# Kernel tuning notes

Measured on AMD Instinct MI355X. Metric: run time of the kernel, lower is better.

Reference implementation:

```python
import jax, jax.numpy as jnp
import numpy as np

D_MODEL = 1024
NUM_HEADS = 16
DFF = 4096
DEPTH = D_MODEL // NUM_HEADS
EPS = 1e-6


def setup_inputs() -> dict:
    key = jax.random.key(0)
    ks = jax.random.split(key, 12)
    B, S, D = 4, 2048, D_MODEL
    scale = 0.02
    inp = {
        "x": jax.random.normal(ks[0], (B, S, D), dtype=jnp.float32),
        "mask": jnp.zeros((B, 1, 1, S), dtype=jnp.float32),
        "wq": jax.random.normal(ks[1], (D, D), dtype=jnp.float32) * scale,
        "bq": jnp.zeros((D,), dtype=jnp.float32),
        "wk": jax.random.normal(ks[2], (D, D), dtype=jnp.float32) * scale,
        "bk": jnp.zeros((D,), dtype=jnp.float32),
        "wv": jax.random.normal(ks[3], (D, D), dtype=jnp.float32) * scale,
        "bv": jnp.zeros((D,), dtype=jnp.float32),
        "wo": jax.random.normal(ks[4], (D, D), dtype=jnp.float32) * scale,
        "bo": jnp.zeros((D,), dtype=jnp.float32),
        "w1": jax.random.normal(ks[5], (D, DFF), dtype=jnp.float32) * scale,
        "b1": jnp.zeros((DFF,), dtype=jnp.float32),
        "w2": jax.random.normal(ks[6], (DFF, D), dtype=jnp.float32) * scale,
        "b2": jnp.zeros((D,), dtype=jnp.float32),
        "g1": jnp.ones((D,), dtype=jnp.float32),
        "beta1": jnp.zeros((D,), dtype=jnp.float32),
        "g2": jnp.ones((D,), dtype=jnp.float32),
        "beta2": jnp.zeros((D,), dtype=jnp.float32),
    }
    return inp


def _layernorm(x, gamma, beta):
    mu = jnp.mean(x, axis=-1, keepdims=True)
    var = jnp.mean(jnp.square(x - mu), axis=-1, keepdims=True)
    return (x - mu) * jax.lax.rsqrt(var + EPS) * gamma + beta


def _split_heads(t, B, S):
    # [B,S,D] -> [B,H,S,depth]
    return t.reshape(B, S, NUM_HEADS, DEPTH).transpose(0, 2, 1, 3)


def encoder_layer(x, mask, wq, bq, wk, bk, wv, bv, wo, bo,
                  w1, b1, w2, b2, g1, beta1, g2, beta2):
    B, S, D = x.shape
    q = _split_heads(x @ wq + bq, B, S)
    k = _split_heads(x @ wk + bk, B, S)
    v = _split_heads(x @ wv + bv, B, S)
    logits = jnp.einsum("bhqd,bhkd->bhqk", q, k) / jnp.sqrt(
        jnp.asarray(DEPTH, dtype=x.dtype))
    if mask is not None:
        logits = logits + mask * -1e9
    attn = jax.nn.softmax(logits, axis=-1)
    ctx = jnp.einsum("bhqk,bhkd->bhqd", attn, v)
    ctx = ctx.transpose(0, 2, 1, 3).reshape(B, S, D)
    attn_out = ctx @ wo + bo
    out1 = _layernorm(x + attn_out, g1, beta1)
    ffn = jax.nn.relu(out1 @ w1 + b1) @ w2 + b2
    out2 = _layernorm(out1 + ffn, g2, beta2)
    return out2


def reference(x, mask, wq, bq, wk, bk, wv, bv, wo, bo,
              w1, b1, w2, b2, g1, beta1, g2, beta2):
    return encoder_layer(x, mask, wq, bq, wk, bk, wv, bv, wo, bo,
                         w1, b1, w2, b2, g1, beta1, g2, beta2)
```

## Files before the change

kernel.cpp:

```cpp
#include <hip/hip_runtime.h>
#include <cstdint>


#define BATCH 4
#define SEQ   2048
#define DM    1024
#define NH    16
#define DEPTH 64
#define DFF_  4096
#define EPSF  1e-6f

typedef short bf16x8 __attribute__((ext_vector_type(8)));
typedef float f32x4  __attribute__((ext_vector_type(4)));

__device__ __forceinline__ unsigned short f2bf(float f) {
  union { float f; unsigned int u; } v; v.f = f;
  unsigned int u = v.u;
  return (unsigned short)((u + 0x7fffu + ((u >> 16) & 1u)) >> 16);
}

__device__ __forceinline__ void gload_lds16(const void* g, void* l) {
  __builtin_amdgcn_global_load_lds(
      (const __attribute__((address_space(1))) unsigned int*)g,
      (__attribute__((address_space(3))) unsigned int*)l, 16, 0, 0);
}

#define VMCNT(n) asm volatile("s_waitcnt vmcnt(" #n ")" ::: "memory")

template<int EPI>
__global__ __launch_bounds__(512, 2)
void gemm8(const unsigned short* __restrict__ A, const unsigned short* __restrict__ Bt,
           const float* __restrict__ bias0, const float* __restrict__ bias1,
           const float* __restrict__ bias2, float* __restrict__ Cf,
           unsigned short* __restrict__ Cb0, unsigned short* __restrict__ Cb1,
           unsigned short* __restrict__ Cb2, int M, int N, int K)
{
  __shared__ char smem[131072];
  const int tid  = threadIdx.x;
  const int lane = tid & 63;
  const int wid  = tid >> 6;
  const int wr   = wid >> 2;
  const int wcn  = wid & 3;
  const int fr   = lane & 15;
  const int kh   = lane >> 4;

  const int nbx  = N >> 8;
  const int nwg  = gridDim.x;
  const int flat = blockIdx.x;
  const int swz  = (flat & 7) * (nwg >> 3) + (flat >> 3);
  const int bx = swz % nbx, by = swz / nbx;
  const int m0 = by << 8, n0 = bx << 8;

  const int lr  = tid >> 3;
  const int ch  = tid & 7;
  const int sch = ch ^ (lr & 7);
  const char* gA = (const char*)A + ((size_t)(m0 + lr) * K) * 2 + sch * 16;
  const char* gB = (const char*)Bt + ((size_t)(n0 + lr) * K) * 2 + sch * 16;
  const size_t rstep = (size_t)K * 128;

  const int chk0 = ((kh) ^ (fr & 7)) * 16;
  const int chk1 = ((4 + kh) ^ (fr & 7)) * 16;
  const int rowA = wr * 128 + fr;
  const int rowB = wcn * 64 + fr;

  f32x4 acc[8][4] = {};
  bf16x8 bg[4][2];
  const int NT = K >> 6;

  {
    char* sb = smem;
    gload_lds16(gB + 0 * rstep, sb + 32768 + 0 * 8192 + tid * 16);
    gload_lds16(gB + 1 * rstep, sb + 32768 + 1 * 8192 + tid * 16);
    gload_lds16(gB + 2 * rstep, sb + 32768 + 2 * 8192 + tid * 16);
    gload_lds16(gB + 3 * rstep, sb + 32768 + 3 * 8192 + tid * 16);
    gload_lds16(gA + 0 * rstep, sb + 0 * 8192 + tid * 16);
    gload_lds16(gA + 2 * rstep, sb + 2 * 8192 + tid * 16);
    gload_lds16(gA + 1 * rstep, sb + 1 * 8192 + tid * 16);
    gload_lds16(gA + 3 * rstep, sb + 3 * 8192 + tid * 16);
    VMCNT(2);
    __builtin_amdgcn_s_barrier();
  }

  for (int t = 0; t < NT - 1; ++t) {
    char* rb = smem + ((t & 1) << 16);
    char* sb = smem + (((t + 1) & 1) << 16);
    const size_t kg = (size_t)(t + 1) * 128;
#pragma unroll
    for (int p = 0; p < 4; ++p) {
      if (p == 0) {
        gload_lds16(gB + kg + 0 * rstep, sb + 32768 + 0 * 8192 + tid * 16);
        gload_lds16(gB + kg + 1 * rstep, sb + 32768 + 1 * 8192 + tid * 16);
      } else if (p == 1) {
        gload_lds16(gB + kg + 2 * rstep, sb + 32768 + 2 * 8192 + tid * 16);
        gload_lds16(gB + kg + 3 * rstep, sb + 32768 + 3 * 8192 + tid * 16);
      } else if (p == 2) {
        gload_lds16(gA + kg + 0 * rstep, sb + 0 * 8192 + tid * 16);
        gload_lds16(gA + kg + 2 * rstep, sb + 2 * 8192 + tid * 16);
      } else {
        gload_lds16(gA + kg + 1 * rstep, sb + 1 * 8192 + tid * 16);
        gload_lds16(gA + kg + 3 * rstep, sb + 3 * 8192 + tid * 16);
      }
      if (p == 0) {
#pragma unroll
        for (int j = 0; j < 4; ++j) {
          bg[j][0] = *(const bf16x8*)(rb + 32768 + (rowB + j * 16) * 128 + chk0);
          bg[j][1] = *(const bf16x8*)(rb + 32768 + (rowB + j * 16) * 128 + chk1);
        }
      }
      bf16x8 a00 = *(const bf16x8*)(rb + (rowA + (2 * p) * 16) * 128 + chk0);
      bf16x8 a01 = *(const bf16x8*)(rb + (rowA + (2 * p) * 16) * 128 + chk1);
      bf16x8 a10 = *(const bf16x8*)(rb + (rowA + (2 * p + 1) * 16) * 128 + chk0);
      bf16x8 a11 = *(const bf16x8*)(rb + (rowA + (2 * p + 1) * 16) * 128 + chk1);
      __builtin_amdgcn_s_barrier();
      __builtin_amdgcn_s_setprio(1);
#pragma unroll
      for (int j = 0; j < 4; ++j) {
        acc[2*p][j]   = __builtin_amdgcn_mfma_f32_16x16x32_bf16(a00, bg[j][0], acc[2*p][j], 0, 0, 0);
        acc[2*p][j]   = __builtin_amdgcn_mfma_f32_16x16x32_bf16(a01, bg[j][1], acc[2*p][j], 0, 0, 0);
        acc[2*p+1][j] = __builtin_amdgcn_mfma_f32_16x16x32_bf16(a10, bg[j][0], acc[2*p+1][j], 0, 0, 0);
        acc[2*p+1][j] = __builtin_amdgcn_mfma_f32_16x16x32_bf16(a11, bg[j][1], acc[2*p+1][j], 0, 0, 0);
      }
      __builtin_amdgcn_s_setprio(0);
      if (p == 1) VMCNT(4);
      if (p == 3) VMCNT(2);
      __builtin_amdgcn_s_barrier();
    }
  }
  {
    char* rb = smem + (((NT - 1) & 1) << 16);
#pragma unroll
    for (int p = 0; p < 4; ++p) {
      if (p == 0) {
#pragma unroll
        for (int j = 0; j < 4; ++j) {
          bg[j][0] = *(const bf16x8*)(rb + 32768 + (rowB + j * 16) * 128 + chk0);
          bg[j][1] = *(const bf16x8*)(rb + 32768 + (rowB + j * 16) * 128 + chk1);
        }
      }
      bf16x8 a00 = *(const bf16x8*)(rb + (rowA + (2 * p) * 16) * 128 + chk0);
      bf16x8 a01 = *(const bf16x8*)(rb + (rowA + (2 * p) * 16) * 128 + chk1);
      bf16x8 a10 = *(const bf16x8*)(rb + (rowA + (2 * p + 1) * 16) * 128 + chk0);
      bf16x8 a11 = *(const bf16x8*)(rb + (rowA + (2 * p + 1) * 16) * 128 + chk1);
      __builtin_amdgcn_s_barrier();
      __builtin_amdgcn_s_setprio(1);
#pragma unroll
      for (int j = 0; j < 4; ++j) {
        acc[2*p][j]   = __builtin_amdgcn_mfma_f32_16x16x32_bf16(a00, bg[j][0], acc[2*p][j], 0, 0, 0);
        acc[2*p][j]   = __builtin_amdgcn_mfma_f32_16x16x32_bf16(a01, bg[j][1], acc[2*p][j], 0, 0, 0);
        acc[2*p+1][j] = __builtin_amdgcn_mfma_f32_16x16x32_bf16(a10, bg[j][0], acc[2*p+1][j], 0, 0, 0);
        acc[2*p+1][j] = __builtin_amdgcn_mfma_f32_16x16x32_bf16(a11, bg[j][1], acc[2*p+1][j], 0, 0, 0);
      }
      __builtin_amdgcn_s_setprio(0);
      if (p == 1) VMCNT(0);
      __builtin_amdgcn_s_barrier();
    }
  }

  if (EPI == 2) {
    const int seg = n0 >> 10;
    const float* bp = seg == 0 ? bias0 : (seg == 1 ? bias1 : bias2);
    unsigned short* dst = seg == 0 ? Cb0 : (seg == 1 ? Cb1 : Cb2);
    float bc[4];
#pragma unroll
    for (int j = 0; j < 4; ++j) bc[j] = bp[(n0 & 1023) + wcn * 64 + j * 16 + fr];
#pragma unroll
    for (int m = 0; m < 8; ++m)
#pragma unroll
      for (int jj = 0; jj < 4; ++jj) {
        const int row = m0 + wr * 128 + m * 16 + kh * 4 + jj;
        const int b = row >> 11, s = row & (SEQ - 1);
#pragma unroll
        for (int j = 0; j < 4; ++j) {
          const int cs = (n0 & 1023) + wcn * 64 + j * 16 + fr;
          const int hh = cs >> 6, d = cs & 63;
          const float v = acc[m][j][jj] + bc[j];
          if (seg < 2)
            dst[(((size_t)(b * NH + hh)) * SEQ + s) * DEPTH + d] = f2bf(v);
          else
            dst[(((size_t)(b * NH + hh)) * DEPTH + d) * SEQ + s] = f2bf(v);
        }
      }
  } else {
    float bc[4];
#pragma unroll
    for (int j = 0; j < 4; ++j) bc[j] = bias0[n0 + wcn * 64 + j * 16 + fr];
#pragma unroll
    for (int m = 0; m < 8; ++m)
#pragma unroll
      for (int jj = 0; jj < 4; ++jj) {
        const int row = m0 + wr * 128 + m * 16 + kh * 4 + jj;
#pragma unroll
        for (int j = 0; j < 4; ++j) {
          const int col = n0 + wcn * 64 + j * 16 + fr;
          float v = acc[m][j][jj] + bc[j];
          if (EPI == 1) {
            v = fmaxf(v, 0.f);
            Cb0[(size_t)row * N + col] = f2bf(v);
          } else {
            Cf[(size_t)row * N + col] = v;
          }
        }
      }
  }
}

template<int EPI>
__global__ __launch_bounds__(512, 2)
void gemm128(const unsigned short* __restrict__ A, const unsigned short* __restrict__ Bt,
             const float* __restrict__ bias0, const float* __restrict__ bias1,
             const float* __restrict__ bias2, float* __restrict__ Cf,
             unsigned short* __restrict__ Cb0, unsigned short* __restrict__ Cb1,
             unsigned short* __restrict__ Cb2, int M, int N, int K)
{
  __shared__ char smem[98304];
  const int tid  = threadIdx.x;
  const int lane = tid & 63;
  const int wid  = tid >> 6;
  const int fr   = lane & 15;
  const int kh   = lane >> 4;

  const int nbx  = N >> 8;
  const int nwg  = gridDim.x;
  const int flat = blockIdx.x;
  const int swz  = (flat & 7) * (nwg >> 3) + (flat >> 3);
  const int bx = swz % nbx, by = swz / nbx;
  const int m0 = by << 7, n0 = bx << 8;

  const int lr  = tid >> 3;
  const int sch = (tid & 7) ^ (lr & 7);
  const char* gA = (const char*)A + ((size_t)(m0 + lr) * K) * 2 + sch * 16;
  const char* gB = (const char*)Bt + ((size_t)(n0 + lr) * K) * 2 + sch * 16;
  const size_t rstep = (size_t)K * 128;

  const int chk0 = ((kh) ^ (fr & 7)) * 16;
  const int chk1 = ((4 + kh) ^ (fr & 7)) * 16;
  const int rowB = wid * 32 + fr;

  f32x4 acc[8][2] = {};
  bf16x8 bg[2][2];
  const int NT = K >> 6;

  {
    char* sb = smem;
    gload_lds16(gB + 0 * rstep, sb + 16384 + 0 * 8192 + tid * 16);
    gload_lds16(gB + 1 * rstep, sb + 16384 + 1 * 8192 + tid * 16);
    gload_lds16(gB + 2 * rstep, sb + 16384 + 2 * 8192 + tid * 16);
    gload_lds16(gB + 3 * rstep, sb + 16384 + 3 * 8192 + tid * 16);
    gload_lds16(gA + 0 * rstep, sb + 0 * 8192 + tid * 16);
    gload_lds16(gA + 1 * rstep, sb + 1 * 8192 + tid * 16);
    VMCNT(1);
    __builtin_amdgcn_s_barrier();
  }

  for (int t = 0; t < NT - 1; ++t) {
    char* rb = smem + (t & 1) * 49152;
    char* sb = smem + ((t + 1) & 1) * 49152;
    const size_t kg = (size_t)(t + 1) * 128;
#pragma unroll
    for (int p = 0; p < 4; ++p) {
      if (p == 0) {
        gload_lds16(gB + kg + 0 * rstep, sb + 16384 + 0 * 8192 + tid * 16);
        gload_lds16(gB + kg + 1 * rstep, sb + 16384 + 1 * 8192 + tid * 16);
      } else if (p == 1) {
        gload_lds16(gB + kg + 2 * rstep, sb + 16384 + 2 * 8192 + tid * 16);
        gload_lds16(gB + kg + 3 * rstep, sb + 16384 + 3 * 8192 + tid * 16);
      } else if (p == 2) {
        gload_lds16(gA + kg + 0 * rstep, sb + 0 * 8192 + tid * 16);
      } else {
        gload_lds16(gA + kg + 1 * rstep, sb + 1 * 8192 + tid * 16);
      }
      if (p == 0) {
#pragma unroll
        for (int j = 0; j < 2; ++j) {
          bg[j][0] = *(const bf16x8*)(rb + 16384 + (rowB + j * 16) * 128 + chk0);
          bg[j][1] = *(const bf16x8*)(rb + 16384 + (rowB + j * 16) * 128 + chk1);
        }
      }
      bf16x8 a00 = *(const bf16x8*)(rb + ((2 * p) * 16 + fr) * 128 + chk0);
      bf16x8 a01 = *(const bf16x8*)(rb + ((2 * p) * 16 + fr) * 128 + chk1);
      bf16x8 a10 = *(const bf16x8*)(rb + ((2 * p + 1) * 16 + fr) * 128 + chk0);
      bf16x8 a11 = *(const bf16x8*)(rb + ((2 * p + 1) * 16 + fr) * 128 + chk1);
      __builtin_amdgcn_s_barrier();
      __builtin_amdgcn_s_setprio(1);
#pragma unroll
      for (int j = 0; j < 2; ++j) {
        acc[2*p][j]   = __builtin_amdgcn_mfma_f32_16x16x32_bf16(a00, bg[j][0], acc[2*p][j], 0, 0, 0);
        acc[2*p][j]   = __builtin_amdgcn_mfma_f32_16x16x32_bf16(a01, bg[j][1], acc[2*p][j], 0, 0, 0);
        acc[2*p+1][j] = __builtin_amdgcn_mfma_f32_16x16x32_bf16(a10, bg[j][0], acc[2*p+1][j], 0, 0, 0);
        acc[2*p+1][j] = __builtin_amdgcn_mfma_f32_16x16x32_bf16(a11, bg[j][1], acc[2*p+1][j], 0, 0, 0);
      }
      __builtin_amdgcn_s_setprio(0);
      if (p == 1) VMCNT(4);
      if (p == 3) VMCNT(1);
      __builtin_amdgcn_s_barrier();
    }
  }
  {
    char* rb = smem + ((NT - 1) & 1) * 49152;
#pragma unroll
    for (int p = 0; p < 4; ++p) {
      if (p == 0) {
#pragma unroll
        for (int j = 0; j < 2; ++j) {
          bg[j][0] = *(const bf16x8*)(rb + 16384 + (rowB + j * 16) * 128 + chk0);
          bg[j][1] = *(const bf16x8*)(rb + 16384 + (rowB + j * 16) * 128 + chk1);
        }
      }
      bf16x8 a00 = *(const bf16x8*)(rb + ((2 * p) * 16 + fr) * 128 + chk0);
      bf16x8 a01 = *(const bf16x8*)(rb + ((2 * p) * 16 + fr) * 128 + chk1);
      bf16x8 a10 = *(const bf16x8*)(rb + ((2 * p + 1) * 16 + fr) * 128 + chk0);
      bf16x8 a11 = *(const bf16x8*)(rb + ((2 * p + 1) * 16 + fr) * 128 + chk1);
      __builtin_amdgcn_s_barrier();
      __builtin_amdgcn_s_setprio(1);
#pragma unroll
      for (int j = 0; j < 2; ++j) {
        acc[2*p][j]   = __builtin_amdgcn_mfma_f32_16x16x32_bf16(a00, bg[j][0], acc[2*p][j], 0, 0, 0);
        acc[2*p][j]   = __builtin_amdgcn_mfma_f32_16x16x32_bf16(a01, bg[j][1], acc[2*p][j], 0, 0, 0);
        acc[2*p+1][j] = __builtin_amdgcn_mfma_f32_16x16x32_bf16(a10, bg[j][0], acc[2*p+1][j], 0, 0, 0);
        acc[2*p+1][j] = __builtin_amdgcn_mfma_f32_16x16x32_bf16(a11, bg[j][1], acc[2*p+1][j], 0, 0, 0);
      }
      __builtin_amdgcn_s_setprio(0);
      if (p == 1) VMCNT(0);
      __builtin_amdgcn_s_barrier();
    }
  }

  if (EPI == 2) {
    const int seg = n0 >> 10;
    const float* bp = seg == 0 ? bias0 : (seg == 1 ? bias1 : bias2);
    unsigned short* dst = seg == 0 ? Cb0 : (seg == 1 ? Cb1 : Cb2);
    float bc[2];
#pragma unroll
    for (int j = 0; j < 2; ++j) bc[j] = bp[(n0 & 1023) + wid * 32 + j * 16 + fr];
#pragma unroll
    for (int m = 0; m < 8; ++m)
#pragma unroll
      for (int jj = 0; jj < 4; ++jj) {
        const int row = m0 + m * 16 + kh * 4 + jj;
        const int b = row >> 11, s = row & (SEQ - 1);
#pragma unroll
        for (int j = 0; j < 2; ++j) {
          const int cs = (n0 & 1023) + wid * 32 + j * 16 + fr;
          const int hh = cs >> 6, d = cs & 63;
          const float v = acc[m][j][jj] + bc[j];
          if (seg < 2)
            dst[(((size_t)(b * NH + hh)) * SEQ + s) * DEPTH + d] = f2bf(v);
          else
            dst[(((size_t)(b * NH + hh)) * DEPTH + d) * SEQ + s] = f2bf(v);
        }
      }
  } else {
    float bc[2];
#pragma unroll
    for (int j = 0; j < 2; ++j) bc[j] = bias0[n0 + wid * 32 + j * 16 + fr];
#pragma unroll
    for (int m = 0; m < 8; ++m)
#pragma unroll
      for (int jj = 0; jj < 4; ++jj) {
        const int row = m0 + m * 16 + kh * 4 + jj;
#pragma unroll
        for (int j = 0; j < 2; ++j) {
          const int col = n0 + wid * 32 + j * 16 + fr;
          Cf[(size_t)row * N + col] = acc[m][j][jj] + bc[j];
        }
      }
  }
}

__global__ __launch_bounds__(256)
void transpose_to_bf16(const float* __restrict__ W, unsigned short* __restrict__ Wt,
                       int K, int N)
{
  __shared__ float t[32][33];
  const int tx = threadIdx.x & 31;
  const int ty = threadIdx.x >> 5;
  const int n0 = blockIdx.x * 32;
  const int k0 = blockIdx.y * 32;
#pragma unroll
  for (int i = 0; i < 4; ++i) {
    int r = ty + i * 8;
    t[r][tx] = W[(size_t)(k0 + r) * N + n0 + tx];
  }
  __syncthreads();
#pragma unroll
  for (int i = 0; i < 4; ++i) {
    int r = ty + i * 8;
    Wt[(size_t)(n0 + r) * K + k0 + tx] = f2bf(t[tx][r]);
  }
}

__global__ __launch_bounds__(256)
void convert_bf16(const float* __restrict__ X, unsigned short* __restrict__ Xb, int n4)
{
  int i = blockIdx.x * 256 + threadIdx.x;
  if (i < n4) {
    float4 v = ((const float4*)X)[i];
    ushort4 r;
    r.x = f2bf(v.x); r.y = f2bf(v.y); r.z = f2bf(v.z); r.w = f2bf(v.w);
    ((ushort4*)Xb)[i] = r;
  }
}

__global__ __launch_bounds__(256)
void attn_mfma(const unsigned short* __restrict__ Qb, const unsigned short* __restrict__ Kb,
               const unsigned short* __restrict__ Vtb, const float* __restrict__ mask,
               unsigned short* __restrict__ ctxb)
{
  __shared__ unsigned short Ks[2][64 * 64];
  __shared__ unsigned short Vts[2][64 * 64];
  __shared__ unsigned short Ps[4][16 * 72];
  __shared__ float Ms[SEQ];

  const int tid  = threadIdx.x;
  const int w    = tid >> 6;
  const int lane = tid & 63;
  const int fr   = lane & 15;
  const int kh   = lane >> 4;
  const int rbase = kh * 4;
  const int bh = blockIdx.y;
  const int b  = bh >> 4, hh = bh & 15;
  const int q0 = blockIdx.x * 64;

  const float MSCL = -1.0e9f * 1.44269504f;
  const float SSCL = 0.125f * 1.44269504f;

  for (int i = tid; i < SEQ / 4; i += 256) {
    float4 mv = *(const float4*)&mask[(size_t)b * SEQ + i * 4];
    mv.x *= MSCL; mv.y *= MSCL; mv.z *= MSCL; mv.w *= MSCL;
    *(float4*)&Ms[i * 4] = mv;
  }

  const size_t qrow = ((size_t)bh * SEQ + q0 + w * 16 + fr) * DEPTH;
  bf16x8 bq[2];
  bq[0] = *(const bf16x8*)(Qb + qrow + kh * 8);
  bq[1] = *(const bf16x8*)(Qb + qrow + 32 + kh * 8);

  float m_run = -1e30f, l_run = 0.f;
  f32x4 o[4] = {};

  const int stg_chunk = (lane & 7) ^ (lane >> 3);
  const int r8 = lane >> 3;
  unsigned short* Pw = &Ps[w][0];

  auto stage = [&](int buf, int kv) {
#pragma unroll
    for (int i = 0; i < 2; ++i) {
      int rr = w * 16 + i * 8 + r8;
      gload_lds16((const char*)Kb + (((size_t)bh * SEQ + kv + rr) * DEPTH) * 2 + stg_chunk * 16,
                  (char*)&Ks[buf][0] + (w * 16 + i * 8) * 128);
      gload_lds16((const char*)Vtb + (((size_t)bh * DEPTH + rr) * SEQ + kv) * 2 + stg_chunk * 16,
                  (char*)&Vts[buf][0] + (w * 16 + i * 8) * 128);
    }
  };

  stage(0, 0);
  __syncthreads();

  int cur = 0;
  for (int kv0 = 0; kv0 < SEQ; kv0 += 64) {
    if (kv0 + 64 < SEQ) stage(cur ^ 1, kv0 + 64);

    const char* kb_ = (const char*)&Ks[cur][0];
    const char* vb_ = (const char*)&Vts[cur][0];

    f32x4 s[4] = {};
#pragma unroll
    for (int ks = 0; ks < 2; ++ks)
#pragma unroll
      for (int j = 0; j < 4; ++j) {
        bf16x8 ak = *(const bf16x8*)(kb_ + (j * 16 + fr) * 128 +
                                     (((ks * 4 + kh) ^ (fr & 7)) * 16));
        s[j] = __builtin_amdgcn_mfma_f32_16x16x32_bf16(ak, bq[ks], s[j], 0, 0, 0);
      }

    float p[16];
    float pmax = -1e30f;
#pragma unroll
    for (int j = 0; j < 4; ++j) {
      float4 mk = *(const float4*)&Ms[kv0 + j * 16 + rbase];
#pragma unroll
      for (int jj = 0; jj < 4; ++jj) {
        float vsc = fmaf(s[j][jj], SSCL, ((const float*)&mk)[jj]);
        p[j * 4 + jj] = vsc;
        pmax = fmaxf(pmax, vsc);
      }
    }
    pmax = fmaxf(pmax, __shfl_xor(pmax, 16));
    pmax = fmaxf(pmax, __shfl_xor(pmax, 32));
    float mnew = fmaxf(m_run, pmax);
    float sc = exp2f(m_run - mnew);
    float rs = 0.f;
#pragma unroll
    for (int t = 0; t < 16; ++t) { p[t] = exp2f(p[t] - mnew); rs += p[t]; }
    rs += __shfl_xor(rs, 16);
    rs += __shfl_xor(rs, 32);
    l_run = l_run * sc + rs;
    m_run = mnew;
#pragma unroll
    for (int db = 0; db < 4; ++db) {
      o[db][0] *= sc; o[db][1] *= sc; o[db][2] *= sc; o[db][3] *= sc;
    }

#pragma unroll
    for (int j = 0; j < 4; ++j) {
      unsigned int lo = (unsigned)f2bf(p[j * 4 + 0]) | ((unsigned)f2bf(p[j * 4 + 1]) << 16);
      unsigned int hi = (unsigned)f2bf(p[j * 4 + 2]) | ((unsigned)f2bf(p[j * 4 + 3]) << 16);
      unsigned long long pk = (unsigned long long)lo | ((unsigned long long)hi << 32);
      *(unsigned long long*)((char*)Pw + fr * 144 + (j * 16 + rbase) * 2) = pk;
    }
#pragma unroll
    for (int ks = 0; ks < 2; ++ks) {
      bf16x8 bp = *(const bf16x8*)((char*)Pw + fr * 144 + ks * 64 + kh * 16);
#pragma unroll
      for (int db = 0; db < 4; ++db) {
        bf16x8 av = *(const bf16x8*)(vb_ + (db * 16 + fr) * 128 +
                                     (((ks * 4 + kh) ^ (fr & 7)) * 16));
        o[db] = __builtin_amdgcn_mfma_f32_16x16x32_bf16(av, bp, o[db], 0, 0, 0);
      }
    }

    VMCNT(0);
    __builtin_amdgcn_s_barrier();
    cur ^= 1;
  }

  float inv = 1.f / l_run;
  const int srow = q0 + w * 16 + fr;
#pragma unroll
  for (int db = 0; db < 4; ++db) {
    ushort4 rb;
    rb.x = f2bf(o[db][0] * inv); rb.y = f2bf(o[db][1] * inv);
    rb.z = f2bf(o[db][2] * inv); rb.w = f2bf(o[db][3] * inv);
    *(ushort4*)(ctxb + ((size_t)(b * SEQ + srow)) * DM + hh * 64 + db * 16 + rbase) = rb;
  }
}

template<int DUAL>
__global__ __launch_bounds__(256)
void add_ln_kernel(const float* __restrict__ X, const float* __restrict__ Y,
                   const float* __restrict__ g, const float* __restrict__ be,
                   float* __restrict__ out, unsigned short* __restrict__ outb)
{
  __shared__ float red[8];
  const int row = blockIdx.x;
  const int tid = threadIdx.x;
  const size_t off = (size_t)row * DM + tid * 4;
  float4 xv = *(const float4*)(X + off);
  float4 yv = *(const float4*)(Y + off);
  float v0 = xv.x + yv.x, v1 = xv.y + yv.y, v2 = xv.z + yv.z, v3 = xv.w + yv.w;
  float s = v0 + v1 + v2 + v3;
#pragma unroll
  for (int m = 1; m < 64; m <<= 1) s += __shfl_xor(s, m);
  if ((tid & 63) == 0) red[tid >> 6] = s;
  __syncthreads();
  float mean = (red[0] + red[1] + red[2] + red[3]) * (1.f / DM);
  float d0 = v0 - mean, d1 = v1 - mean, d2 = v2 - mean, d3 = v3 - mean;
  float sq = d0 * d0 + d1 * d1 + d2 * d2 + d3 * d3;
#pragma unroll
  for (int m = 1; m < 64; m <<= 1) sq += __shfl_xor(sq, m);
  if ((tid & 63) == 0) red[4 + (tid >> 6)] = sq;
  __syncthreads();
  float var = (red[4] + red[5] + red[6] + red[7]) * (1.f / DM);
  float inv = rsqrtf(var + EPSF);
  int col = tid * 4;
  float4 r;
  r.x = d0 * inv * g[col + 0] + be[col + 0];
  r.y = d1 * inv * g[col + 1] + be[col + 1];
  r.z = d2 * inv * g[col + 2] + be[col + 2];
  r.w = d3 * inv * g[col + 3] + be[col + 3];
  *(float4*)(out + off) = r;
  if (DUAL) {
    ushort4 rb;
    rb.x = f2bf(r.x); rb.y = f2bf(r.y); rb.z = f2bf(r.z); rb.w = f2bf(r.w);
    *(ushort4*)(outb + off) = rb;
  }
}

extern "C" void kernel_launch(void* const* d_in, const int* in_sizes, int n_in,
                              void* d_out, int out_size, void* d_ws, size_t ws_size,
                              hipStream_t stream)
{
  const float* x    = (const float*)d_in[0];
  const float* mask = (const float*)d_in[1];
  const float* wq   = (const float*)d_in[2];
  const float* bq   = (const float*)d_in[3];
  const float* wk   = (const float*)d_in[4];
  const float* bk   = (const float*)d_in[5];
  const float* wv   = (const float*)d_in[6];
  const float* bv   = (const float*)d_in[7];
  const float* wo   = (const float*)d_in[8];
  const float* bo   = (const float*)d_in[9];
  const float* w1   = (const float*)d_in[10];
  const float* b1   = (const float*)d_in[11];
  const float* w2   = (const float*)d_in[12];
  const float* b2   = (const float*)d_in[13];
  const float* g1   = (const float*)d_in[14];
  const float* be1  = (const float*)d_in[15];
  const float* g2   = (const float*)d_in[16];
  const float* be2  = (const float*)d_in[17];
  float* out = (float*)d_out;
  char* wsb = (char*)d_ws;

  unsigned short* qb    = (unsigned short*)(wsb);
  unsigned short* kb    = (unsigned short*)(wsb + (16u << 20));
  unsigned short* vtb   = (unsigned short*)(wsb + (32u << 20));
  unsigned short* ctxb  = (unsigned short*)(wsb + (48u << 20));
  unsigned short* xb    = (unsigned short*)(wsb + (64u << 20));
  unsigned short* hbuf  = (unsigned short*)(wsb + (80u << 20));
  unsigned short* wqkvt = (unsigned short*)(wsb + (144u << 20));
  unsigned short* wot   = (unsigned short*)(wsb + (150u << 20));
  unsigned short* w1t   = (unsigned short*)(wsb + (152u << 20));
  unsigned short* w2t   = (unsigned short*)(wsb + (160u << 20));
  float* attn_out = (float*)(wsb);
  float* out1     = (float*)(wsb + (32u << 20));
  unsigned short* out1b = xb;
  float* ffn      = (float*)(wsb);

  dim3 blk(256);
  const int M = BATCH * SEQ;

  convert_bf16<<<8192, blk, 0, stream>>>(x, xb, (BATCH * SEQ * DM) / 4);
  transpose_to_bf16<<<dim3(32, 32), blk, 0, stream>>>(wq, wqkvt, DM, DM);
  transpose_to_bf16<<<dim3(32, 32), blk, 0, stream>>>(wk, wqkvt + 1024 * 1024, DM, DM);
  transpose_to_bf16<<<dim3(32, 32), blk, 0, stream>>>(wv, wqkvt + 2 * 1024 * 1024, DM, DM);
  transpose_to_bf16<<<dim3(32, 32), blk, 0, stream>>>(wo, wot, DM, DM);
  transpose_to_bf16<<<dim3(128, 32), blk, 0, stream>>>(w1, w1t, DM, DFF_);
  transpose_to_bf16<<<dim3(32, 128), blk, 0, stream>>>(w2, w2t, DFF_, DM);

  gemm128<2><<<dim3((M / 128) * (3072 / 256)), dim3(512), 0, stream>>>(
      xb, wqkvt, bq, bk, bv, nullptr, qb, kb, vtb, M, 3072, DM);

  attn_mfma<<<dim3(SEQ / 64, BATCH * NH), blk, 0, stream>>>(qb, kb, vtb, mask, ctxb);

  gemm128<0><<<dim3((M / 128) * (DM / 256)), dim3(512), 0, stream>>>(
      ctxb, wot, bo, nullptr, nullptr, attn_out, nullptr, nullptr, nullptr, M, DM, DM);
  add_ln_kernel<1><<<dim3(M), blk, 0, stream>>>(x, attn_out, g1, be1, out1, out1b);

  gemm8<1><<<dim3((M / 256) * (DFF_ / 256)), dim3(512), 0, stream>>>(
      out1b, w1t, b1, nullptr, nullptr, nullptr, hbuf, nullptr, nullptr, M, DFF_, DM);
  gemm128<0><<<dim3((M / 128) * (DM / 256)), dim3(512), 0, stream>>>(
      hbuf, w2t, b2, nullptr, nullptr, ffn, nullptr, nullptr, nullptr, M, DM, DFF_);

  add_ln_kernel<0><<<dim3(M), blk, 0, stream>>>(out1, ffn, g2, be2, out, nullptr);
}
```

Measured before the change: 639.4 us.

## Restructure GEMM k-loop into two halves and simplify attention loop with lazy rescale

Result: faster. 614.4 us (-3.9%).

```diff
diff --git a/kernel.cpp b/kernel.cpp
--- a/kernel.cpp
+++ b/kernel.cpp
@@ -1,4 +1,5 @@
 #include <hip/hip_runtime.h>
+#include <hip/hip_bf16.h>
 #include <cstdint>
 
 
@@ -17,6 +18,11 @@
   union { float f; unsigned int u; } v; v.f = f;
   unsigned int u = v.u;
   return (unsigned short)((u + 0x7fffu + ((u >> 16) & 1u)) >> 16);
+}
+
+__device__ __forceinline__ unsigned pkbf(float a, float b) {
+  __hip_bfloat162 h = __float22bfloat162_rn(make_float2(a, b));
+  unsigned u; __builtin_memcpy(&u, &h, 4); return u;
 }
 
 __device__ __forceinline__ void gload_lds16(const void* g, void* l) {
@@ -52,8 +58,7 @@
   const int m0 = by << 8, n0 = bx << 8;
 
   const int lr  = tid >> 3;
-  const int ch  = tid & 7;
-  const int sch = ch ^ (lr & 7);
+  const int sch = (tid & 7) ^ (lr & 7);
   const char* gA = (const char*)A + ((size_t)(m0 + lr) * K) * 2 + sch * 16;
   const char* gB = (const char*)Bt + ((size_t)(n0 + lr) * K) * 2 + sch * 16;
   const size_t rstep = (size_t)K * 128;
@@ -256,72 +261,101 @@
     char* rb = smem + (t & 1) * 49152;
     char* sb = smem + ((t + 1) & 1) * 49152;
     const size_t kg = (size_t)(t + 1) * 128;
-#pragma unroll
-    for (int p = 0; p < 4; ++p) {
-      if (p == 0) {
-        gload_lds16(gB + kg + 0 * rstep, sb + 16384 + 0 * 8192 + tid * 16);
-        gload_lds16(gB + kg + 1 * rstep, sb + 16384 + 1 * 8192 + tid * 16);
-      } else if (p == 1) {
-        gload_lds16(gB + kg + 2 * rstep, sb + 16384 + 2 * 8192 + tid * 16);
-        gload_lds16(gB + kg + 3 * rstep, sb + 16384 + 3 * 8192 + tid * 16);
-      } else if (p == 2) {
-        gload_lds16(gA + kg + 0 * rstep, sb + 0 * 8192 + tid * 16);
-      } else {
-        gload_lds16(gA + kg + 1 * rstep, sb + 1 * 8192 + tid * 16);
-      }
-      if (p == 0) {
+
+    gload_lds16(gB + kg + 0 * rstep, sb + 16384 + 0 * 8192 + tid * 16);
+    gload_lds16(gB + kg + 1 * rstep, sb + 16384 + 1 * 8192 + tid * 16);
+    gload_lds16(gB + kg + 2 * rstep, sb + 16384 + 2 * 8192 + tid * 16);
+#pragma unroll
+    for (int j = 0; j < 2; ++j) {
+      bg[j][0] = *(const bf16x8*)(rb + 16384 + (rowB + j * 16) * 128 + chk0);
+      bg[j][1] = *(const bf16x8*)(rb + 16384 + (rowB + j * 16) * 128 + chk1);
+    }
+    {
+      bf16x8 a[4][2];
+#pragma unroll
+      for (int m = 0; m < 4; ++m) {
+        a[m][0] = *(const bf16x8*)(rb + ((m * 16 + fr) * 128) + chk0);
+        a[m][1] = *(const bf16x8*)(rb + ((m * 16 + fr) * 128) + chk1);
+      }
+      __builtin_amdgcn_s_barrier();
+      __builtin_amdgcn_s_setprio(1);
+#pragma unroll
+      for (int m = 0; m < 4; ++m)
 #pragma unroll
         for (int j = 0; j < 2; ++j) {
-          bg[j][0] = *(const bf16x8*)(rb + 16384 + (rowB + j * 16) * 128 + chk0);
-          bg[j][1] = *(const bf16x8*)(rb + 16384 + (rowB + j * 16) * 128 + chk1);
-        }
-      }
-      bf16x8 a00 = *(const bf16x8*)(rb + ((2 * p) * 16 + fr) * 128 + chk0);
-      bf16x8 a01 = *(const bf16x8*)(rb + ((2 * p) * 16 + fr) * 128 + chk1);
-      bf16x8 a10 = *(const bf16x8*)(rb + ((2 * p + 1) * 16 + fr) * 128 + chk0);
-      bf16x8 a11 = *(const bf16x8*)(rb + ((2 * p + 1) * 16 + fr) * 128 + chk1);
+          acc[m][j] = __builtin_amdgcn_mfma_f32_16x16x32_bf16(a[m][0], bg[j][0], acc[m][j], 0, 0, 0);
+          acc[m][j] = __builtin_amdgcn_mfma_f32_16x16x32_bf16(a[m][1], bg[j][1], acc[m][j], 0, 0, 0);
+        }
+      __builtin_amdgcn_s_setprio(0);
+      VMCNT(3);
+      __builtin_amdgcn_s_barrier();
+    }
+
+    gload_lds16(gB + kg + 3 * rstep, sb + 16384 + 3 * 8192 + tid * 16);
+    gload_lds16(gA + kg + 0 * rstep, sb + 0 * 8192 + tid * 16);
+    gload_lds16(gA + kg + 1 * rstep, sb + 1 * 8192 + tid * 16);
+    {
+      bf16x8 a[4][2];
+#pragma unroll
+      for (int m = 0; m < 4; ++m) {
+        a[m][0] = *(const bf16x8*)(rb + (((m + 4) * 16 + fr) * 128) + chk0);
+        a[m][1] = *(const bf16x8*)(rb + (((m + 4) * 16 + fr) * 128) + chk1);
+      }
       __builtin_amdgcn_s_barrier();
       __builtin_amdgcn_s_setprio(1);
 #pragma unroll
-      for (int j = 0; j < 2; ++j) {
-        acc[2*p][j]   = __builtin_amdgcn_mfma_f32_16x16x32_bf16(a00, bg[j][0], acc[2*p][j], 0, 0, 0);
-        acc[2*p][j]   = __builtin_amdgcn_mfma_f32_16x16x32_bf16(a01, bg[j][1], acc[2*p][j], 0, 0, 0);
-        acc[2*p+1][j] = __builtin_amdgcn_mfma_f32_16x16x32_bf16(a10, bg[j][0], acc[2*p+1][j], 0, 0, 0);
-        acc[2*p+1][j] = __builtin_amdgcn_mfma_f32_16x16x32_bf16(a11, bg[j][1], acc[2*p+1][j], 0, 0, 0);
-      }
+      for (int m = 0; m < 4; ++m)
+#pragma unroll
+        for (int j = 0; j < 2; ++j) {
+          acc[m+4][j] = __builtin_amdgcn_mfma_f32_16x16x32_bf16(a[m][0], bg[j][0], acc[m+4][j], 0, 0, 0);
+          acc[m+4][j] = __builtin_amdgcn_mfma_f32_16x16x32_bf16(a[m][1], bg[j][1], acc[m+4][j], 0, 0, 0);
+        }
       __builtin_amdgcn_s_setprio(0);
-      if (p == 1) VMCNT(4);
-      if (p == 3) VMCNT(1);
+      VMCNT(1);
       __builtin_amdgcn_s_barrier();
     }
   }
   {
     char* rb = smem + ((NT - 1) & 1) * 49152;
 #pragma unroll
-    for (int p = 0; p < 4; ++p) {
-      if (p == 0) {
+    for (int j = 0; j < 2; ++j) {
+      bg[j][0] = *(const bf16x8*)(rb + 16384 + (rowB + j * 16) * 128 + chk0);
+      bg[j][1] = *(const bf16x8*)(rb + 16384 + (rowB + j * 16) * 128 + chk1);
+    }
+    {
+      bf16x8 a[4][2];
+#pragma unroll
+      for (int m = 0; m < 4; ++m) {
+        a[m][0] = *(const bf16x8*)(rb + ((m * 16 + fr) * 128) + chk0);
+        a[m][1] = *(const bf16x8*)(rb + ((m * 16 + fr) * 128) + chk1);
+      }
+      __builtin_amdgcn_s_barrier();
+      __builtin_amdgcn_s_setprio(1);
+#pragma unroll
+      for (int m = 0; m < 4; ++m)
 #pragma unroll
         for (int j = 0; j < 2; ++j) {
-          bg[j][0] = *(const bf16x8*)(rb + 16384 + (rowB + j * 16) * 128 + chk0);
-          bg[j][1] = *(const bf16x8*)(rb + 16384 + (rowB + j * 16) * 128 + chk1);
-        }
-      }
-      bf16x8 a00 = *(const bf16x8*)(rb + ((2 * p) * 16 + fr) * 128 + chk0);
-      bf16x8 a01 = *(const bf16x8*)(rb + ((2 * p) * 16 + fr) * 128 + chk1);
-      bf16x8 a10 = *(const bf16x8*)(rb + ((2 * p + 1) * 16 + fr) * 128 + chk0);
-      bf16x8 a11 = *(const bf16x8*)(rb + ((2 * p + 1) * 16 + fr) * 128 + chk1);
-      __builtin_amdgcn_s_barrier();
-      __builtin_amdgcn_s_setprio(1);
-#pragma unroll
-      for (int j = 0; j < 2; ++j) {
-        acc[2*p][j]   = __builtin_amdgcn_mfma_f32_16x16x32_bf16(a00, bg[j][0], acc[2*p][j], 0, 0, 0);
-        acc[2*p][j]   = __builtin_amdgcn_mfma_f32_16x16x32_bf16(a01, bg[j][1], acc[2*p][j], 0, 0, 0);
-        acc[2*p+1][j] = __builtin_amdgcn_mfma_f32_16x16x32_bf16(a10, bg[j][0], acc[2*p+1][j], 0, 0, 0);
-        acc[2*p+1][j] = __builtin_amdgcn_mfma_f32_16x16x32_bf16(a11, bg[j][1], acc[2*p+1][j], 0, 0, 0);
-      }
+          acc[m][j] = __builtin_amdgcn_mfma_f32_16x16x32_bf16(a[m][0], bg[j][0], acc[m][j], 0, 0, 0);
+          acc[m][j] = __builtin_amdgcn_mfma_f32_16x16x32_bf16(a[m][1], bg[j][1], acc[m][j], 0, 0, 0);
+        }
       __builtin_amdgcn_s_setprio(0);
-      if (p == 1) VMCNT(0);
-      __builtin_amdgcn_s_barrier();
+      VMCNT(0);
+      __builtin_amdgcn_s_barrier();
+    }
+    {
+      bf16x8 a[4][2];
+#pragma unroll
+      for (int m = 0; m < 4; ++m) {
+        a[m][0] = *(const bf16x8*)(rb + (((m + 4) * 16 + fr) * 128) + chk0);
+        a[m][1] = *(const bf16x8*)(rb + (((m + 4) * 16 + fr) * 128) + chk1);
+      }
+#pragma unroll
+      for (int m = 0; m < 4; ++m)
+#pragma unroll
+        for (int j = 0; j < 2; ++j) {
+          acc[m+4][j] = __builtin_amdgcn_mfma_f32_16x16x32_bf16(a[m][0], bg[j][0], acc[m+4][j], 0, 0, 0);
+          acc[m+4][j] = __builtin_amdgcn_mfma_f32_16x16x32_bf16(a[m][1], bg[j][1], acc[m+4][j], 0, 0, 0);
+        }
     }
   }
 
@@ -406,10 +440,9 @@
                const unsigned short* __restrict__ Vtb, const float* __restrict__ mask,
                unsigned short* __restrict__ ctxb)
 {
-  __shared__ unsigned short Ks[2][64 * 64];
-  __shared__ unsigned short Vts[2][64 * 64];
+  __shared__ unsigned short Ks[64 * 64];
+  __shared__ unsigned short Vts[64 * 64];
   __shared__ unsigned short Ps[4][16 * 72];
-  __shared__ float Ms[SEQ];
 
   const int tid  = threadIdx.x;
   const int w    = tid >> 6;
@@ -424,12 +457,6 @@
   const float MSCL = -1.0e9f * 1.44269504f;
   const float SSCL = 0.125f * 1.44269504f;
 
-  for (int i = tid; i < SEQ / 4; i += 256) {
-    float4 mv = *(const float4*)&mask[(size_t)b * SEQ + i * 4];
-    mv.x *= MSCL; mv.y *= MSCL; mv.z *= MSCL; mv.w *= MSCL;
-    *(float4*)&Ms[i * 4] = mv;
-  }
-
   const size_t qrow = ((size_t)bh * SEQ + q0 + w * 16 + fr) * DEPTH;
   bf16x8 bq[2];
   bq[0] = *(const bf16x8*)(Qb + qrow + kh * 8);
@@ -441,87 +468,82 @@
   const int stg_chunk = (lane & 7) ^ (lane >> 3);
   const int r8 = lane >> 3;
   unsigned short* Pw = &Ps[w][0];
-
-  auto stage = [&](int buf, int kv) {
+  const float* mrow = mask + (size_t)b * SEQ;
+
+  for (int kv0 = 0; kv0 < SEQ; kv0 += 64) {
+    __syncthreads();
 #pragma unroll
     for (int i = 0; i < 2; ++i) {
       int rr = w * 16 + i * 8 + r8;
-      gload_lds16((const char*)Kb + (((size_t)bh * SEQ + kv + rr) * DEPTH) * 2 + stg_chunk * 16,
-                  (char*)&Ks[buf][0] + (w * 16 + i * 8) * 128);
-      gload_lds16((const char*)Vtb + (((size_t)bh * DEPTH + rr) * SEQ + kv) * 2 + stg_chunk * 16,
-                  (char*)&Vts[buf][0] + (w * 16 + i * 8) * 128);
-    }
-  };
-
-  stage(0, 0);
-  __syncthreads();
-
-  int cur = 0;
-  for (int kv0 = 0; kv0 < SEQ; kv0 += 64) {
-    if (kv0 + 64 < SEQ) stage(cur ^ 1, kv0 + 64);
-
-    const char* kb_ = (const char*)&Ks[cur][0];
-    const char* vb_ = (const char*)&Vts[cur][0];
+      gload_lds16((const char*)Kb + (((size_t)bh * SEQ + kv0 + rr) * DEPTH) * 2 + stg_chunk * 16,
+                  (char*)Ks + (w * 16 + i * 8) * 128);
+      gload_lds16((const char*)Vtb + (((size_t)bh * DEPTH + rr) * SEQ + kv0) * 2 + stg_chunk * 16,
+                  (char*)Vts + (w * 16 + i * 8) * 128);
+    }
+    __syncthreads();
 
     f32x4 s[4] = {};
+    __builtin_amdgcn_s_setprio(1);
 #pragma unroll
     for (int ks = 0; ks < 2; ++ks)
 #pragma unroll
       for (int j = 0; j < 4; ++j) {
-        bf16x8 ak = *(const bf16x8*)(kb_ + (j * 16 + fr) * 128 +
+        bf16x8 ak = *(const bf16x8*)((const char*)Ks + (j * 16 + fr) * 128 +
                                      (((ks * 4 + kh) ^ (fr & 7)) * 16));
         s[j] = __builtin_amdgcn_mfma_f32_16x16x32_bf16(ak, bq[ks], s[j], 0, 0, 0);
       }
+    __builtin_amdgcn_s_setprio(0);
 
     float p[16];
     float pmax = -1e30f;
 #pragma unroll
     for (int j = 0; j < 4; ++j) {
-      float4 mk = *(const float4*)&Ms[kv0 + j * 16 + rbase];
+      float4 mk = *(const float4*)&mrow[kv0 + j * 16 + rbase];
 #pragma unroll
       for (int jj = 0; jj < 4; ++jj) {
-        float vsc = fmaf(s[j][jj], SSCL, ((const float*)&mk)[jj]);
+        float vsc = fmaf(((const float*)&mk)[jj], MSCL, s[j][jj] * SSCL);
         p[j * 4 + jj] = vsc;
         pmax = fmaxf(pmax, vsc);
       }
     }
     pmax = fmaxf(pmax, __shfl_xor(pmax, 16));
     pmax = fmaxf(pmax, __shfl_xor(pmax, 32));
-    float mnew = fmaxf(m_run, pmax);
-    float sc = exp2f(m_run - mnew);
+    if (!__all(pmax - m_run <= 8.f)) {
+      float mnew = fmaxf(m_run, pmax);
+      float sc = __builtin_amdgcn_exp2f(m_run - mnew);
+      l_run *= sc;
+      m_run = mnew;
+#pragma unroll
+      for (int db = 0; db < 4; ++db) {
+        o[db][0] *= sc; o[db][1] *= sc; o[db][2] *= sc; o[db][3] *= sc;
+      }
+    }
     float rs = 0.f;
 #pragma unroll
-    for (int t = 0; t < 16; ++t) { p[t] = exp2f(p[t] - mnew); rs += p[t]; }
+    for (int t = 0; t < 16; ++t) { p[t] = __builtin_amdgcn_exp2f(p[t] - m_run); rs += p[t]; }
     rs += __shfl_xor(rs, 16);
     rs += __shfl_xor(rs, 32);
-    l_run = l_run * sc + rs;
-    m_run = mnew;
-#pragma unroll
-    for (int db = 0; db < 4; ++db) {
-      o[db][0] *= sc; o[db][1] *= sc; o[db][2] *= sc; o[db][3] *= sc;
-    }
+    l_run += rs;
 
 #pragma unroll
     for (int j = 0; j < 4; ++j) {
-      unsigned int lo = (unsigned)f2bf(p[j * 4 + 0]) | ((unsigned)f2bf(p[j * 4 + 1]) << 16);
-      unsigned int hi = (unsigned)f2bf(p[j * 4 + 2]) | ((unsigned)f2bf(p[j * 4 + 3]) << 16);
+      unsigned int lo = pkbf(p[j * 4 + 0], p[j * 4 + 1]);
+      unsigned int hi = pkbf(p[j * 4 + 2], p[j * 4 + 3]);
       unsigned long long pk = (unsigned long long)lo | ((unsigned long long)hi << 32);
       *(unsigned long long*)((char*)Pw + fr * 144 + (j * 16 + rbase) * 2) = pk;
     }
+    __builtin_amdgcn_s_setprio(1);
 #pragma unroll
     for (int ks = 0; ks < 2; ++ks) {
       bf16x8 bp = *(const bf16x8*)((char*)Pw + fr * 144 + ks * 64 + kh * 16);
 #pragma unroll
       for (int db = 0; db < 4; ++db) {
-        bf16x8 av = *(const bf16x8*)(vb_ + (db * 16 + fr) * 128 +
+        bf16x8 av = *(const bf16x8*)((const char*)Vts + (db * 16 + fr) * 128 +
                                      (((ks * 4 + kh) ^ (fr & 7)) * 16));
         o[db] = __builtin_amdgcn_mfma_f32_16x16x32_bf16(av, bp, o[db], 0, 0, 0);
       }
     }
-
-    VMCNT(0);
-    __builtin_amdgcn_s_barrier();
-    cur ^= 1;
+    __builtin_amdgcn_s_setprio(0);
   }
 
   float inv = 1.f / l_run;
```
